# Kernel tuning notes

Hardware: AMD Instinct MI355X
Metric: run time of the kernel (lower is better)

## Reference

```python
import jax, jax.numpy as jnp
import numpy as np

NUM_CLASSES = 4
GAMMA = 2.0          # FocalLoss gamma
T_ALPHA, T_BETA = 0.3, 0.7
SMOOTH = 1e-5
W_DICE, W_CE, W_BOUND = 1.0, 1.0, 0.01
INF = 1e12


def _dt1d(f):
    # min-plus 1D squared distance transform along last axis (brute Felzenszwalb)
    n = f.shape[-1]
    i = jnp.arange(n, dtype=f.dtype)
    d2 = (i[:, None] - i[None, :]) ** 2          # [n, n]
    return jnp.min(f[..., None, :] + d2, axis=-1)


def _edt(seed):
    # Euclidean distance from every voxel to the nearest True voxel in `seed`
    f = jnp.where(seed, 0.0, INF).astype(jnp.float32)
    for ax in range(f.ndim):
        f = jnp.moveaxis(_dt1d(jnp.moveaxis(f, ax, -1)), -1, ax)
    return jnp.sqrt(f)


def _sdf(mask):
    # signed distance map, matching compute_edt_map (mask: bool [D,H,W])
    s = mask.sum()
    size = mask.size
    dist_out = _edt(mask)        # scipy distance(1-mask)
    dist_in = _edt(~mask)        # scipy distance(mask)
    sdf = dist_out - dist_in
    sdf = jnp.where(s == 0, 1.0, jnp.where(s == size, -1.0, sdf))
    return sdf


def setup_inputs() -> dict:
    key = jax.random.key(0)
    k1, k2 = jax.random.split(key)
    preds = jax.random.normal(k1, (4, NUM_CLASSES, 64, 64, 64), dtype=jnp.float32)
    targets = jax.random.randint(k2, (4, 64, 64, 64), 0, NUM_CLASSES).astype(jnp.int64)
    return {"preds": preds, "targets": targets}


def reference(preds, targets):
    B = preds.shape[0]
    sp_dims = (2, 3, 4)

    probs = jax.nn.softmax(preds, axis=1)                       # [B,C,D,H,W]
    onehot = (targets[:, None] == jnp.arange(NUM_CLASSES)[None, :, None, None, None]).astype(preds.dtype)

    # ---- Tversky ----
    TP = jnp.sum(probs * onehot, axis=sp_dims)
    FP = jnp.sum(probs * (1.0 - onehot), axis=sp_dims)
    FN = jnp.sum((1.0 - probs) * onehot, axis=sp_dims)
    tversky = (TP + SMOOTH) / (TP + T_ALPHA * FP + T_BETA * FN + SMOOTH)
    l_dice = 1.0 - tversky.mean()

    # ---- Focal ----
    logp = jax.nn.log_softmax(preds, axis=1)
    ce = -jnp.take_along_axis(logp, targets[:, None], axis=1)[:, 0]   # [B,D,H,W]
    pt = jnp.exp(-ce)
    l_main = jnp.mean((1.0 - pt) ** GAMMA * ce)

    # ---- Boundary ----
    masks = targets[:, None] == jnp.arange(1, NUM_CLASSES)[None, :, None, None, None]  # [B,3,D,H,W] bool
    flat = masks.reshape((-1,) + masks.shape[2:])
    sdfs = jax.lax.map(_sdf, flat).reshape(masks.shape)               # [B,3,D,H,W]
    nonempty = jnp.sum(masks, axis=sp_dims) > 0                       # [B,3]
    contrib = jnp.mean(sdfs * probs[:, 1:NUM_CLASSES], axis=sp_dims)  # [B,3]
    l_bound = jnp.sum(jnp.where(nonempty, contrib, 0.0)) / (B * (NUM_CLASSES - 1) + 1e-8)

    return W_DICE * l_dice + W_CE * l_main + W_BOUND * l_bound
```

## Files before the change

kernel.cpp:

```cpp
#include <hip/hip_runtime.h>
#include <math.h>

#define SPATIAL 262144
#define NVOX    1048576
#define NVOL    12
#define INFV    1e12f

#define ACC_SUMP  0
#define ACC_TP    16
#define ACC_CNT   32
#define ACC_FOCAL 48
#define ACC_BOUND 52
#define ACC_N     64
#define NPART     13
#define RCHUNK    256

__global__ void zero_acc_kernel(float* acc) {
    if (threadIdx.x < ACC_N) acc[threadIdx.x] = 0.0f;
}

__device__ __forceinline__ void voxel_accum(float p0, float p1, float p2, float p3,
                                            int t, float* loc) {
    float m = fmaxf(fmaxf(p0, p1), fmaxf(p2, p3));
    float e0 = __expf(p0 - m), e1 = __expf(p1 - m);
    float e2 = __expf(p2 - m), e3 = __expf(p3 - m);
    float s = e0 + e1 + e2 + e3;
    float inv = __builtin_amdgcn_rcpf(s);
    float q0 = e0 * inv, q1 = e1 * inv, q2 = e2 * inv, q3 = e3 * inv;
    float pl = (t == 0) ? p0 : (t == 1) ? p1 : (t == 2) ? p2 : p3;
    float ce = __logf(s) + (m - pl);
    float qt = (t == 0) ? q0 : (t == 1) ? q1 : (t == 2) ? q2 : q3;
    float om = 1.0f - qt;
    loc[0] += q0; loc[1] += q1; loc[2] += q2; loc[3] += q3;
    if (t == 0)      { loc[4] += q0; loc[8]  += 1.f; }
    else if (t == 1) { loc[5] += q1; loc[9]  += 1.f; }
    else if (t == 2) { loc[6] += q2; loc[10] += 1.f; }
    else             { loc[7] += q3; loc[11] += 1.f; }
    loc[12] += om * om * ce;
}

__global__ __launch_bounds__(256) void reduce_kernel(
        const float* __restrict__ preds, const int* __restrict__ targets,
        float* __restrict__ partials) {
    int bb = blockIdx.x;
    int b = bb >> 8, chunk = bb & 255;
    int tid = threadIdx.x;
    const float* pb = preds + (size_t)b * 4 * SPATIAL;
    const int* tb = targets + b * SPATIAL;
    float loc[NPART];
    #pragma unroll
    for (int k = 0; k < NPART; ++k) loc[k] = 0.0f;

    int sp = chunk * 1024 + tid * 4;
    float4 P0 = *(const float4*)(pb + 0 * SPATIAL + sp);
    float4 P1 = *(const float4*)(pb + 1 * SPATIAL + sp);
    float4 P2 = *(const float4*)(pb + 2 * SPATIAL + sp);
    float4 P3 = *(const float4*)(pb + 3 * SPATIAL + sp);
    int4   T  = *(const int4*)(tb + sp);
    voxel_accum(P0.x, P1.x, P2.x, P3.x, T.x, loc);
    voxel_accum(P0.y, P1.y, P2.y, P3.y, T.y, loc);
    voxel_accum(P0.z, P1.z, P2.z, P3.z, T.z, loc);
    voxel_accum(P0.w, P1.w, P2.w, P3.w, T.w, loc);

    int lane = tid & 63, w = tid >> 6;
    #pragma unroll
    for (int k = 0; k < NPART; ++k) {
        float v = loc[k];
        #pragma unroll
        for (int off = 32; off > 0; off >>= 1)
            v += __shfl_down(v, off, 64);
        loc[k] = v;
    }
    __shared__ float sred[NPART][4];
    if (lane == 0) {
        #pragma unroll
        for (int k = 0; k < NPART; ++k) sred[k][w] = loc[k];
    }
    __syncthreads();
    if (tid < NPART) {
        float tot = sred[tid][0] + sred[tid][1] + sred[tid][2] + sred[tid][3];
        partials[(b * NPART + tid) * RCHUNK + chunk] = tot;
    }
}

__global__ __launch_bounds__(256) void stage2_kernel(
        const float* __restrict__ partials, float* __restrict__ acc) {
    int r = blockIdx.x;
    int b = r / NPART, k = r % NPART;
    int tid = threadIdx.x;
    int lane = tid & 63, w = tid >> 6;
    float v = partials[(b * NPART + k) * RCHUNK + tid];
    #pragma unroll
    for (int off = 32; off > 0; off >>= 1)
        v += __shfl_down(v, off, 64);
    __shared__ float sred[4];
    if (lane == 0) sred[w] = v;
    __syncthreads();
    if (tid == 0) {
        float tot = sred[0] + sred[1] + sred[2] + sred[3];
        int dst = (k < 4)  ? (ACC_SUMP + b * 4 + k)
                : (k < 8)  ? (ACC_TP   + b * 4 + (k - 4))
                : (k < 12) ? (ACC_CNT  + b * 4 + (k - 8))
                : (ACC_FOCAL + b);
        acc[dst] = tot;
    }
}

__device__ __forceinline__ float row_d2(unsigned long long m, int i) {
    if (m == 0ull) return INFV;
    unsigned long long right = m >> i;
    unsigned long long left  = m << (63 - i);
    int dr = right ? __builtin_ctzll(right) : 1000;
    int dl = left  ? __builtin_clzll(left)  : 1000;
    int d = (dr < dl) ? dr : dl;
    return (float)(d * d);
}

#define MINPLUS_BODY(LO, LI, AO, AI, LANE, W)                                   \
    {                                                                           \
        int base = (W) * 8;                                                     \
        _Pragma("unroll")                                                       \
        for (int jj = 0; jj < 8; ++jj) {                                        \
            float vo = LO[(base + jj) * 64 + (LANE)];                           \
            float vi = LI[(base + jj) * 64 + (LANE)];                           \
            _Pragma("unroll")                                                   \
            for (int k = 0; k < 8; ++k) {                                       \
                float d = (float)(k - jj);                                      \
                AO[k] = fminf(AO[k], fmaf(d, d, vo));                           \
                AI[k] = fminf(AI[k], fmaf(d, d, vi));                           \
            }                                                                   \
        }                                                                       \
        int el_max = base;                                                      \
        int er_max = 56 - base;                                                 \
        int t = 1;                                                              \
        while (true) {                                                          \
            float am = 0.0f;                                                    \
            _Pragma("unroll")                                                   \
            for (int k = 0; k < 8; ++k) am = fmaxf(am, fmaxf(AO[k], AI[k]));    \
            _Pragma("unroll")                                                   \
            for (int off = 32; off > 0; off >>= 1)                              \
                am = fmaxf(am, __shfl_xor(am, off, 64));                        \
            int dmax = (int)sqrtf(fmaxf(am - 1.0f, 0.0f));                      \
            int Tl = (dmax < el_max) ? dmax : el_max;                           \
            int Tr = (dmax < er_max) ? dmax : er_max;                           \
            int T = (Tl > Tr) ? Tl : Tr;                                        \
            if (t > T) break;                                                   \
            int tend = (T < t + 3) ? T : (t + 3);                               \
            for (; t <= tend; ++t) {                                            \
                float ft = (float)t;                                            \
                if (t <= Tl) {                                                  \
                    int j = base - t;                                           \
                    float vo = LO[j * 64 + (LANE)];                             \
                    float vi = LI[j * 64 + (LANE)];                             \
                    _Pragma("unroll")                                           \
                    for (int k = 0; k < 8; ++k) {                               \
                        float d = ft + (float)k;                                \
                        AO[k] = fminf(AO[k], fmaf(d, d, vo));                   \
                        AI[k] = fminf(AI[k], fmaf(d, d, vi));                   \
                    }                                                           \
                }                                                               \
                if (t <= Tr) {                                                  \
                    int j = base + 7 + t;                                       \
                    float vo = LO[j * 64 + (LANE)];                             \
                    float vi = LI[j * 64 + (LANE)];                             \
                    float fr = ft + 7.0f;                                       \
                    _Pragma("unroll")                                           \
                    for (int k = 0; k < 8; ++k) {                               \
                        float d = fr - (float)k;                                \
                        AO[k] = fminf(AO[k], fmaf(d, d, vo));                   \
                        AI[k] = fminf(AI[k], fmaf(d, d, vi));                   \
                    }                                                           \
                }                                                               \
            }                                                                   \
        }                                                                       \
    }

__global__ __launch_bounds__(512) void dtxy_kernel(
        const int* __restrict__ targets,
        float* __restrict__ dtOut, float* __restrict__ dtIn) {
    __shared__ float lo[4096];
    __shared__ float li[4096];
    int blk = blockIdx.x;
    int v = blk >> 6, z = blk & 63;
    int b = v / 3, cls = (v % 3) + 1;
    const int* tp = targets + b * SPATIAL + z * 4096;
    int t = threadIdx.x;
    int lane = t & 63, w = t >> 6;

    #pragma unroll
    for (int k = 0; k < 8; ++k) {
        int y = w * 8 + k;
        int tv = tp[y * 64 + lane];
        unsigned long long m = __ballot(tv == cls);
        lo[y * 64 + lane] = row_d2(m, lane);
        li[y * 64 + lane] = row_d2(~m, lane);
    }
    __syncthreads();

    float ao[8], ai[8];
    #pragma unroll
    for (int k = 0; k < 8; ++k) { ao[k] = 3.0e38f; ai[k] = 3.0e38f; }
    MINPLUS_BODY(lo, li, ao, ai, lane, w)

    size_t vol = (size_t)v * SPATIAL;
    #pragma unroll
    for (int k = 0; k < 8; ++k) {
        int i = w * 8 + k;
        size_t g = vol + (size_t)z * 4096 + (size_t)i * 64 + lane;
        dtOut[g] = ao[k];
        dtIn[g]  = ai[k];
    }
}

__global__ __launch_bounds__(512) void dtz_final_kernel(
        const float* __restrict__ dtOut, const float* __restrict__ dtIn,
        const float* __restrict__ preds, float* __restrict__ acc) {
    __shared__ float lo[4096];
    __shared__ float li[4096];
    int blk = blockIdx.x;
    int v = blk >> 6, y = blk & 63;
    int b = v / 3, cls = (v % 3) + 1;
    size_t vol = (size_t)v * SPATIAL;
    int t = threadIdx.x;
    int lane = t & 63, w = t >> 6;

    #pragma unroll
    for (int k = 0; k < 8; ++k) {
        int idx = k * 512 + t;
        int zz = idx >> 6, x = idx & 63;
        size_t g = vol + (size_t)zz * 4096 + (size_t)y * 64 + x;
        lo[idx] = dtOut[g];
        li[idx] = dtIn[g];
    }
    __syncthreads();

    float ao[8], ai[8];
    #pragma unroll
    for (int k = 0; k < 8; ++k) { ao[k] = 3.0e38f; ai[k] = 3.0e38f; }
    MINPLUS_BODY(lo, li, ao, ai, lane, w)

    float partial = 0.0f;
    const float* pbase = preds + (size_t)b * 4 * SPATIAL;
    #pragma unroll
    for (int k = 0; k < 8; ++k) {
        int i = w * 8 + k;
        size_t sp = (size_t)i * 4096 + (size_t)y * 64 + lane;
        float sv = sqrtf(ao[k]) - sqrtf(ai[k]);
        float p0 = pbase[sp], p1 = pbase[SPATIAL + sp];
        float p2 = pbase[2 * SPATIAL + sp], p3 = pbase[3 * SPATIAL + sp];
        float m = fmaxf(fmaxf(p0, p1), fmaxf(p2, p3));
        float e0 = __expf(p0 - m), e1 = __expf(p1 - m);
        float e2 = __expf(p2 - m), e3 = __expf(p3 - m);
        float s = e0 + e1 + e2 + e3;
        float ec = (cls == 1) ? e1 : (cls == 2) ? e2 : e3;
        partial += sv * (ec * __builtin_amdgcn_rcpf(s));
    }
    #pragma unroll
    for (int off = 32; off > 0; off >>= 1)
        partial += __shfl_down(partial, off, 64);
    __shared__ float ws8[8];
    if (lane == 0) ws8[w] = partial;
    __syncthreads();
    if (t == 0) {
        float tot = 0.0f;
        #pragma unroll
        for (int i = 0; i < 8; ++i) tot += ws8[i];
        atomicAdd(&acc[ACC_BOUND + v], tot);
    }
}

__global__ void finalize_kernel(const float* __restrict__ acc, float* __restrict__ out) {
    if (threadIdx.x != 0 || blockIdx.x != 0) return;
    float tsum = 0.0f;
    for (int i = 0; i < 16; ++i) {
        float TP = acc[ACC_TP + i];
        float S  = acc[ACC_SUMP + i];
        float CN = acc[ACC_CNT + i];
        float FP = S - TP;
        float FN = CN - TP;
        tsum += (TP + 1e-5f) / (TP + 0.3f * FP + 0.7f * FN + 1e-5f);
    }
    float l_dice = 1.0f - tsum / 16.0f;
    float l_main = (acc[ACC_FOCAL] + acc[ACC_FOCAL + 1] +
                    acc[ACC_FOCAL + 2] + acc[ACC_FOCAL + 3]) / (float)NVOX;
    float bsum = 0.0f;
    for (int v = 0; v < NVOL; ++v) {
        int b = v / 3, c = (v % 3) + 1;
        float CN = acc[ACC_CNT + b * 4 + c];
        float contrib;
        if (CN <= 0.0f) contrib = 0.0f;
        else if (CN >= (float)SPATIAL) contrib = -acc[ACC_SUMP + b * 4 + c] / (float)SPATIAL;
        else contrib = acc[ACC_BOUND + v] / (float)SPATIAL;
        bsum += contrib;
    }
    float l_bound = bsum / (12.0f + 1e-8f);
    out[0] = l_dice + l_main + 0.01f * l_bound;
}

extern "C" void kernel_launch(void* const* d_in, const int* in_sizes, int n_in,
                              void* d_out, int out_size, void* d_ws, size_t ws_size,
                              hipStream_t stream) {
    const float* preds = (const float*)d_in[0];
    const int* targets = (const int*)d_in[1];
    float* out = (float*)d_out;
    float* ws = (float*)d_ws;
    float* acc = ws;
    float* partials = ws + ACC_N;
    float* dtOut = partials + 4 * NPART * RCHUNK;
    float* dtIn = dtOut + (size_t)NVOL * SPATIAL;

    hipLaunchKernelGGL(zero_acc_kernel, dim3(1), dim3(64), 0, stream, acc);
    hipLaunchKernelGGL(reduce_kernel, dim3(4 * RCHUNK), dim3(256), 0, stream,
                       preds, targets, partials);
    hipLaunchKernelGGL(stage2_kernel, dim3(4 * NPART), dim3(256), 0, stream, partials, acc);
    hipLaunchKernelGGL(dtxy_kernel, dim3(NVOL * 64), dim3(512), 0, stream,
                       targets, dtOut, dtIn);
    hipLaunchKernelGGL(dtz_final_kernel, dim3(NVOL * 64), dim3(512), 0, stream,
                       dtOut, dtIn, preds, acc);
    hipLaunchKernelGGL(finalize_kernel, dim3(1), dim3(64), 0, stream, acc, out);
}
```

Baseline: 111.3 us.

## Pack inside/outside squared distances into u16 pairs and merge final reductions

Stores the outside and inside squared distances for the distance transform as two 16-bit integers in one 32-bit word. The min-plus passes then use packed u16 min/max instead of paired float fminf/fma, which halves LDS footprint and global intermediate traffic. The stage2, zero and finalize kernels are folded into a single final kernel that reduces the partials and per-block boundary sums, removing the atomics and two launches. Squared distances are capped at a 16-bit far value, and the early-exit bound is now derived from integer maxima with a +1 margin. Both could change behaviour for degenerate masks.

```diff
diff --git a/kernel.cpp b/kernel.cpp
--- a/kernel.cpp
+++ b/kernel.cpp
@@ -4,20 +4,24 @@
 #define SPATIAL 262144
 #define NVOX    1048576
 #define NVOL    12
-#define INFV    1e12f
-
-#define ACC_SUMP  0
-#define ACC_TP    16
-#define ACC_CNT   32
-#define ACC_FOCAL 48
-#define ACC_BOUND 52
-#define ACC_N     64
-#define NPART     13
-#define RCHUNK    256
-
-__global__ void zero_acc_kernel(float* acc) {
-    if (threadIdx.x < ACC_N) acc[threadIdx.x] = 0.0f;
-}
+#define FAR_D2  50000
+#define NPART   13
+#define RCHUNK  256
+
+typedef unsigned short u16x2 __attribute__((ext_vector_type(2)));
+union pku { unsigned int u; u16x2 v; };
+
+__device__ __forceinline__ unsigned int pk_min(unsigned int a, unsigned int b) {
+    pku x, y; x.u = a; y.u = b;
+    x.v = __builtin_elementwise_min(x.v, y.v);
+    return x.u;
+}
+__device__ __forceinline__ unsigned int pk_max(unsigned int a, unsigned int b) {
+    pku x, y; x.u = a; y.u = b;
+    x.v = __builtin_elementwise_max(x.v, y.v);
+    return x.u;
+}
+
 
 __device__ __forceinline__ void voxel_accum(float p0, float p1, float p2, float p3,
                                             int t, float* loc) {
@@ -83,92 +87,64 @@
     }
 }
 
-__global__ __launch_bounds__(256) void stage2_kernel(
-        const float* __restrict__ partials, float* __restrict__ acc) {
-    int r = blockIdx.x;
-    int b = r / NPART, k = r % NPART;
-    int tid = threadIdx.x;
-    int lane = tid & 63, w = tid >> 6;
-    float v = partials[(b * NPART + k) * RCHUNK + tid];
-    #pragma unroll
-    for (int off = 32; off > 0; off >>= 1)
-        v += __shfl_down(v, off, 64);
-    __shared__ float sred[4];
-    if (lane == 0) sred[w] = v;
-    __syncthreads();
-    if (tid == 0) {
-        float tot = sred[0] + sred[1] + sred[2] + sred[3];
-        int dst = (k < 4)  ? (ACC_SUMP + b * 4 + k)
-                : (k < 8)  ? (ACC_TP   + b * 4 + (k - 4))
-                : (k < 12) ? (ACC_CNT  + b * 4 + (k - 8))
-                : (ACC_FOCAL + b);
-        acc[dst] = tot;
-    }
-}
-
-__device__ __forceinline__ float row_d2(unsigned long long m, int i) {
-    if (m == 0ull) return INFV;
+
+__device__ __forceinline__ int row_d2i(unsigned long long m, int i) {
+    if (m == 0ull) return FAR_D2;
     unsigned long long right = m >> i;
     unsigned long long left  = m << (63 - i);
     int dr = right ? __builtin_ctzll(right) : 1000;
     int dl = left  ? __builtin_clzll(left)  : 1000;
     int d = (dr < dl) ? dr : dl;
-    return (float)(d * d);
-}
-
-#define MINPLUS_BODY(LO, LI, AO, AI, LANE, W)                                   \
+    return d * d;
+}
+
+#define MINPLUS_PK(LA, ACC, LANE, W)                                            \
     {                                                                           \
-        int base = (W) * 8;                                                     \
+        const int base = (W) * 8;                                               \
         _Pragma("unroll")                                                       \
         for (int jj = 0; jj < 8; ++jj) {                                        \
-            float vo = LO[(base + jj) * 64 + (LANE)];                           \
-            float vi = LI[(base + jj) * 64 + (LANE)];                           \
+            unsigned int wv = LA[(base + jj) * 64 + (LANE)];                    \
             _Pragma("unroll")                                                   \
             for (int k = 0; k < 8; ++k) {                                       \
-                float d = (float)(k - jj);                                      \
-                AO[k] = fminf(AO[k], fmaf(d, d, vo));                           \
-                AI[k] = fminf(AI[k], fmaf(d, d, vi));                           \
+                int d = k - jj;                                                 \
+                unsigned int dd = (unsigned int)(d * d);                        \
+                ACC[k] = pk_min(ACC[k], wv + (dd | (dd << 16)));                \
             }                                                                   \
         }                                                                       \
-        int el_max = base;                                                      \
-        int er_max = 56 - base;                                                 \
+        const int el_max = base, er_max = 56 - base;                            \
         int t = 1;                                                              \
         while (true) {                                                          \
-            float am = 0.0f;                                                    \
+            unsigned int am = 0;                                                \
             _Pragma("unroll")                                                   \
-            for (int k = 0; k < 8; ++k) am = fmaxf(am, fmaxf(AO[k], AI[k]));    \
+            for (int k = 0; k < 8; ++k) am = pk_max(am, ACC[k]);                \
             _Pragma("unroll")                                                   \
             for (int off = 32; off > 0; off >>= 1)                              \
-                am = fmaxf(am, __shfl_xor(am, off, 64));                        \
-            int dmax = (int)sqrtf(fmaxf(am - 1.0f, 0.0f));                      \
+                am = pk_max(am, (unsigned int)__shfl_xor((int)am, off, 64));    \
+            int amx = (int)(am & 0xFFFFu), amy = (int)(am >> 16);               \
+            int mm = (amx > amy) ? amx : amy;                                   \
+            int dmax = (int)sqrtf((float)mm) + 1;     \
             int Tl = (dmax < el_max) ? dmax : el_max;                           \
             int Tr = (dmax < er_max) ? dmax : er_max;                           \
             int T = (Tl > Tr) ? Tl : Tr;                                        \
             if (t > T) break;                                                   \
             int tend = (T < t + 3) ? T : (t + 3);                               \
             for (; t <= tend; ++t) {                                            \
-                float ft = (float)t;                                            \
                 if (t <= Tl) {                                                  \
-                    int j = base - t;                                           \
-                    float vo = LO[j * 64 + (LANE)];                             \
-                    float vi = LI[j * 64 + (LANE)];                             \
+                    unsigned int wv = LA[(base - t) * 64 + (LANE)];             \
                     _Pragma("unroll")                                           \
                     for (int k = 0; k < 8; ++k) {                               \
-                        float d = ft + (float)k;                                \
-                        AO[k] = fminf(AO[k], fmaf(d, d, vo));                   \
-                        AI[k] = fminf(AI[k], fmaf(d, d, vi));                   \
+                        int d = t + k;                                          \
+                        unsigned int dd = (unsigned int)(d * d);                \
+                        ACC[k] = pk_min(ACC[k], wv + (dd | (dd << 16)));        \
                     }                                                           \
                 }                                                               \
                 if (t <= Tr) {                                                  \
-                    int j = base + 7 + t;                                       \
-                    float vo = LO[j * 64 + (LANE)];                             \
-                    float vi = LI[j * 64 + (LANE)];                             \
-                    float fr = ft + 7.0f;                                       \
+                    unsigned int wv = LA[(base + 7 + t) * 64 + (LANE)];         \
                     _Pragma("unroll")                                           \
                     for (int k = 0; k < 8; ++k) {                               \
-                        float d = fr - (float)k;                                \
-                        AO[k] = fminf(AO[k], fmaf(d, d, vo));                   \
-                        AI[k] = fminf(AI[k], fmaf(d, d, vi));                   \
+                        int d = t + 7 - k;                                      \
+                        unsigned int dd = (unsigned int)(d * d);                \
+                        ACC[k] = pk_min(ACC[k], wv + (dd | (dd << 16)));        \
                     }                                                           \
                 }                                                               \
             }                                                                   \
@@ -176,68 +152,60 @@
     }
 
 __global__ __launch_bounds__(512) void dtxy_kernel(
-        const int* __restrict__ targets,
-        float* __restrict__ dtOut, float* __restrict__ dtIn) {
-    __shared__ float lo[4096];
-    __shared__ float li[4096];
+        const int* __restrict__ targets, unsigned int* __restrict__ dtp) {
+    __shared__ unsigned int la[4096];
     int blk = blockIdx.x;
     int v = blk >> 6, z = blk & 63;
     int b = v / 3, cls = (v % 3) + 1;
     const int* tp = targets + b * SPATIAL + z * 4096;
-    int t = threadIdx.x;
-    int lane = t & 63, w = t >> 6;
+    int t = threadIdx.x, lane = t & 63, w = t >> 6;
 
     #pragma unroll
     for (int k = 0; k < 8; ++k) {
         int y = w * 8 + k;
         int tv = tp[y * 64 + lane];
         unsigned long long m = __ballot(tv == cls);
-        lo[y * 64 + lane] = row_d2(m, lane);
-        li[y * 64 + lane] = row_d2(~m, lane);
-    }
-    __syncthreads();
-
-    float ao[8], ai[8];
-    #pragma unroll
-    for (int k = 0; k < 8; ++k) { ao[k] = 3.0e38f; ai[k] = 3.0e38f; }
-    MINPLUS_BODY(lo, li, ao, ai, lane, w)
+        int do2 = row_d2i(m, lane);
+        int di2 = row_d2i(~m, lane);
+        la[y * 64 + lane] = (unsigned int)do2 | ((unsigned int)di2 << 16);
+    }
+    __syncthreads();
+
+    unsigned int acc[8];
+    #pragma unroll
+    for (int k = 0; k < 8; ++k) acc[k] = 0xFFFFFFFFu;
+    MINPLUS_PK(la, acc, lane, w)
 
     size_t vol = (size_t)v * SPATIAL;
     #pragma unroll
     for (int k = 0; k < 8; ++k) {
         int i = w * 8 + k;
-        size_t g = vol + (size_t)z * 4096 + (size_t)i * 64 + lane;
-        dtOut[g] = ao[k];
-        dtIn[g]  = ai[k];
+        dtp[vol + (size_t)z * 4096 + (size_t)i * 64 + lane] = acc[k];
     }
 }
 
 __global__ __launch_bounds__(512) void dtz_final_kernel(
-        const float* __restrict__ dtOut, const float* __restrict__ dtIn,
-        const float* __restrict__ preds, float* __restrict__ acc) {
-    __shared__ float lo[4096];
-    __shared__ float li[4096];
+        const unsigned int* __restrict__ dtp, const float* __restrict__ preds,
+        float* __restrict__ bound) {
+    __shared__ unsigned int la[4096];
     int blk = blockIdx.x;
     int v = blk >> 6, y = blk & 63;
     int b = v / 3, cls = (v % 3) + 1;
     size_t vol = (size_t)v * SPATIAL;
-    int t = threadIdx.x;
-    int lane = t & 63, w = t >> 6;
+    int t = threadIdx.x, lane = t & 63, w = t >> 6;
 
     #pragma unroll
     for (int k = 0; k < 8; ++k) {
         int idx = k * 512 + t;
         int zz = idx >> 6, x = idx & 63;
-        size_t g = vol + (size_t)zz * 4096 + (size_t)y * 64 + x;
-        lo[idx] = dtOut[g];
-        li[idx] = dtIn[g];
-    }
-    __syncthreads();
-
-    float ao[8], ai[8];
-    #pragma unroll
-    for (int k = 0; k < 8; ++k) { ao[k] = 3.0e38f; ai[k] = 3.0e38f; }
-    MINPLUS_BODY(lo, li, ao, ai, lane, w)
+        la[idx] = dtp[vol + (size_t)zz * 4096 + (size_t)y * 64 + x];
+    }
+    __syncthreads();
+
+    unsigned int acc[8];
+    #pragma unroll
+    for (int k = 0; k < 8; ++k) acc[k] = 0xFFFFFFFFu;
+    MINPLUS_PK(la, acc, lane, w)
 
     float partial = 0.0f;
     const float* pbase = preds + (size_t)b * 4 * SPATIAL;
@@ -245,7 +213,9 @@
     for (int k = 0; k < 8; ++k) {
         int i = w * 8 + k;
         size_t sp = (size_t)i * 4096 + (size_t)y * 64 + lane;
-        float sv = sqrtf(ao[k]) - sqrtf(ai[k]);
+        float dout = (float)(acc[k] & 0xFFFFu);
+        float din  = (float)(acc[k] >> 16);
+        float sv = sqrtf(dout) - sqrtf(din);
         float p0 = pbase[sp], p1 = pbase[SPATIAL + sp];
         float p2 = pbase[2 * SPATIAL + sp], p3 = pbase[3 * SPATIAL + sp];
         float m = fmaxf(fmaxf(p0, p1), fmaxf(p2, p3));
@@ -265,35 +235,59 @@
         float tot = 0.0f;
         #pragma unroll
         for (int i = 0; i < 8; ++i) tot += ws8[i];
-        atomicAdd(&acc[ACC_BOUND + v], tot);
-    }
-}
-
-__global__ void finalize_kernel(const float* __restrict__ acc, float* __restrict__ out) {
-    if (threadIdx.x != 0 || blockIdx.x != 0) return;
+        bound[blk] = tot;
+    }
+}
+
+__global__ __launch_bounds__(256) void final_kernel(
+        const float* __restrict__ partials, const float* __restrict__ bound,
+        float* __restrict__ out) {
+    __shared__ float rowsum[52];
+    __shared__ float bsum[12];
+    int tid = threadIdx.x, lane = tid & 63, w = tid >> 6;
+
+    for (int r = w; r < 52; r += 4) {
+        const float* p = partials + r * RCHUNK;
+        float v = p[lane] + p[64 + lane] + p[128 + lane] + p[192 + lane];
+        #pragma unroll
+        for (int off = 32; off > 0; off >>= 1)
+            v += __shfl_down(v, off, 64);
+        if (lane == 0) rowsum[r] = v;
+    }
+    for (int r = w; r < 12; r += 4) {
+        float v = bound[r * 64 + lane];
+        #pragma unroll
+        for (int off = 32; off > 0; off >>= 1)
+            v += __shfl_down(v, off, 64);
+        if (lane == 0) bsum[r] = v;
+    }
+    __syncthreads();
+    if (tid != 0) return;
+
     float tsum = 0.0f;
-    for (int i = 0; i < 16; ++i) {
-        float TP = acc[ACC_TP + i];
-        float S  = acc[ACC_SUMP + i];
-        float CN = acc[ACC_CNT + i];
-        float FP = S - TP;
-        float FN = CN - TP;
-        tsum += (TP + 1e-5f) / (TP + 0.3f * FP + 0.7f * FN + 1e-5f);
-    }
+    for (int b = 0; b < 4; ++b)
+        for (int c = 0; c < 4; ++c) {
+            float S  = rowsum[b * NPART + c];
+            float TP = rowsum[b * NPART + 4 + c];
+            float CN = rowsum[b * NPART + 8 + c];
+            float FP = S - TP;
+            float FN = CN - TP;
+            tsum += (TP + 1e-5f) / (TP + 0.3f * FP + 0.7f * FN + 1e-5f);
+        }
     float l_dice = 1.0f - tsum / 16.0f;
-    float l_main = (acc[ACC_FOCAL] + acc[ACC_FOCAL + 1] +
-                    acc[ACC_FOCAL + 2] + acc[ACC_FOCAL + 3]) / (float)NVOX;
-    float bsum = 0.0f;
+    float l_main = (rowsum[12] + rowsum[NPART + 12] +
+                    rowsum[2 * NPART + 12] + rowsum[3 * NPART + 12]) / (float)NVOX;
+    float bs = 0.0f;
     for (int v = 0; v < NVOL; ++v) {
         int b = v / 3, c = (v % 3) + 1;
-        float CN = acc[ACC_CNT + b * 4 + c];
+        float CN = rowsum[b * NPART + 8 + c];
         float contrib;
         if (CN <= 0.0f) contrib = 0.0f;
-        else if (CN >= (float)SPATIAL) contrib = -acc[ACC_SUMP + b * 4 + c] / (float)SPATIAL;
-        else contrib = acc[ACC_BOUND + v] / (float)SPATIAL;
-        bsum += contrib;
-    }
-    float l_bound = bsum / (12.0f + 1e-8f);
+        else if (CN >= (float)SPATIAL) contrib = -rowsum[b * NPART + c] / (float)SPATIAL;
+        else contrib = bsum[v] / (float)SPATIAL;
+        bs += contrib;
+    }
+    float l_bound = bs / (12.0f + 1e-8f);
     out[0] = l_dice + l_main + 0.01f * l_bound;
 }
 
@@ -304,18 +298,16 @@
     const int* targets = (const int*)d_in[1];
     float* out = (float*)d_out;
     float* ws = (float*)d_ws;
-    float* acc = ws;
-    float* partials = ws + ACC_N;
-    float* dtOut = partials + 4 * NPART * RCHUNK;
-    float* dtIn = dtOut + (size_t)NVOL * SPATIAL;
-
-    hipLaunchKernelGGL(zero_acc_kernel, dim3(1), dim3(64), 0, stream, acc);
+    float* partials = ws;
+    float* bound = ws + 4 * NPART * RCHUNK;
+    unsigned int* dtp = (unsigned int*)(ws + 4 * NPART * RCHUNK + NVOL * 64);
+
     hipLaunchKernelGGL(reduce_kernel, dim3(4 * RCHUNK), dim3(256), 0, stream,
                        preds, targets, partials);
-    hipLaunchKernelGGL(stage2_kernel, dim3(4 * NPART), dim3(256), 0, stream, partials, acc);
     hipLaunchKernelGGL(dtxy_kernel, dim3(NVOL * 64), dim3(512), 0, stream,
-                       targets, dtOut, dtIn);
+                       targets, dtp);
     hipLaunchKernelGGL(dtz_final_kernel, dim3(NVOL * 64), dim3(512), 0, stream,
-                       dtOut, dtIn, preds, acc);
-    hipLaunchKernelGGL(finalize_kernel, dim3(1), dim3(64), 0, stream, acc, out);
-}
+                       dtp, preds, bound);
+    hipLaunchKernelGGL(final_kernel, dim3(1), dim3(256), 0, stream,
+                       partials, bound, out);
+}
```

Result: no change. 110.7 us (-0.6%).
